# Kernel optimization log

Measured on AMD Instinct MI355X. Metric: run time of the kernel, lower is better.

Reference implementation:

```python
import jax, jax.numpy as jnp
import numpy as np

N = 50000      # nodes
E = 800000     # edges (avg degree 16)
D_IN = 128     # node_feature_dim
H = 256        # hidden_dim
EPS = 1e-5     # BatchNorm eps


def setup_inputs() -> dict:
    key = jax.random.key(0)
    ks = jax.random.split(key, 32)
    inp = {
        "x": jax.random.normal(ks[0], (N, D_IN), jnp.float32),
        "edge_index": jax.random.randint(ks[1], (2, E), 0, N, jnp.int32),
    }
    dims = [(D_IN, H), (H, H), (H, H)]
    k = 2
    for i, (din, dout) in enumerate(dims):
        s = 1.0 / np.sqrt(din)
        inp[f"Wl{i}"] = jax.random.uniform(ks[k], (din, dout), jnp.float32, -s, s); k += 1
        inp[f"bl{i}"] = jax.random.uniform(ks[k], (dout,), jnp.float32, -s, s); k += 1
        inp[f"Wr{i}"] = jax.random.uniform(ks[k], (din, dout), jnp.float32, -s, s); k += 1
        inp[f"g{i}"] = jnp.ones((dout,), jnp.float32)
        inp[f"b{i}"] = jnp.zeros((dout,), jnp.float32)
        inp[f"rm{i}"] = jax.random.normal(ks[k], (dout,), jnp.float32) * 0.1; k += 1
        inp[f"rv{i}"] = jax.random.uniform(ks[k], (dout,), jnp.float32, 0.5, 1.5); k += 1
    return inp


def _sage(x, src, dst, Wl, bl, Wr):
    # PyG SAGEConv (aggr='mean'): out = lin_l(mean_{j in N(i)} x_j) + lin_r(x_i)
    deg = jax.ops.segment_sum(jnp.ones((src.shape[0],), x.dtype), dst, num_segments=N)
    agg = jax.ops.segment_sum(x[src], dst, num_segments=N)  # [N, d_in]
    mean = agg / jnp.maximum(deg, 1.0)[:, None]
    return mean @ Wl + bl + x @ Wr


def _bn(x, g, b, rm, rv):
    # eval-mode BatchNorm1d with running stats
    return (x - rm) * (g * jax.lax.rsqrt(rv + EPS)) + b


def reference(x, edge_index,
              Wl0, bl0, Wr0, g0, b0, rm0, rv0,
              Wl1, bl1, Wr1, g1, b1, rm1, rv1,
              Wl2, bl2, Wr2, g2, b2, rm2, rv2):
    src, dst = edge_index[0], edge_index[1]
    h = jax.nn.relu(_bn(_sage(x, src, dst, Wl0, bl0, Wr0), g0, b0, rm0, rv0))
    h = jax.nn.relu(_bn(_sage(h, src, dst, Wl1, bl1, Wr1), g1, b1, rm1, rv1))
    h = _bn(_sage(h, src, dst, Wl2, bl2, Wr2), g2, b2, rm2, rv2)
    return h  # [N, H] node embeddings (dropout is identity in eval mode)
```

## Files before the change

kernel.cpp:

```cpp
#include <hip/hip_runtime.h>
#include <hip/hip_bf16.h>

#define NNODES 50000
#define NEDGES 800000
#define HID 256
#define BN_EPS 1e-5f
#define SCAN_B ((NNODES + 255) / 256)

typedef __attribute__((ext_vector_type(8))) short short8v;
typedef __attribute__((ext_vector_type(4))) float f32x4;
typedef __attribute__((ext_vector_type(2))) float f32x2;

__device__ inline void load_lds16(const void* g, void* l) {
    __builtin_amdgcn_global_load_lds(
        (const __attribute__((address_space(1))) unsigned int*)g,
        (__attribute__((address_space(3))) unsigned int*)l, 16, 0, 0);
}

__global__ void k_countrank(const int* __restrict__ ei, int* __restrict__ cnt,
                            int* __restrict__ rank, int nE) {
    int e = blockIdx.x * blockDim.x + threadIdx.x;
    if (e < nE) rank[e] = atomicAdd(&cnt[ei[nE + e]], 1);
}

__global__ void k_bsum(const int* __restrict__ cnt, int* __restrict__ loc,
                       int* __restrict__ bsum, int n) {
    __shared__ int sh[256];
    int tid = threadIdx.x;
    int i = blockIdx.x * 256 + tid;
    int v = (i < n) ? cnt[i] : 0;
    sh[tid] = v;
    __syncthreads();
    for (int off = 1; off < 256; off <<= 1) {
        int t = (tid >= off) ? sh[tid - off] : 0;
        __syncthreads();
        sh[tid] += t;
        __syncthreads();
    }
    if (i < n) loc[i] = sh[tid] - v;
    if (tid == 255) bsum[blockIdx.x] = sh[255];
}

__global__ void k_bscan(int* __restrict__ bsum, int nb) {
    __shared__ int sh[256];
    int tid = threadIdx.x;
    int v = (tid < nb) ? bsum[tid] : 0;
    sh[tid] = v;
    __syncthreads();
    for (int off = 1; off < 256; off <<= 1) {
        int t = (tid >= off) ? sh[tid - off] : 0;
        __syncthreads();
        sh[tid] += t;
        __syncthreads();
    }
    if (tid < nb) bsum[tid] = sh[tid] - v;
}

__global__ void k_addoff(const int* __restrict__ loc, const int* __restrict__ bsum,
                         int* __restrict__ rowptr, int n, int nE) {
    int i = blockIdx.x * 256 + threadIdx.x;
    if (i < n) rowptr[i] = loc[i] + bsum[blockIdx.x];
    if (i == 0) rowptr[n] = nE;
}

__global__ void k_fill2(const int* __restrict__ ei, const int* __restrict__ rowptr,
                        const int* __restrict__ rank, int* __restrict__ col, int nE) {
    int e = blockIdx.x * blockDim.x + threadIdx.x;
    if (e < nE) col[rowptr[ei[nE + e]] + rank[e]] = ei[e];
}

#define PREP_CAST 1600000
#define PREP_TR   327680
__global__ void k_prep(const float* __restrict__ x,
                       __hip_bfloat16* __restrict__ xb, unsigned char* __restrict__ x8,
                       const float* __restrict__ s0, const float* __restrict__ s1,
                       const float* __restrict__ s2, const float* __restrict__ s3,
                       const float* __restrict__ s4, const float* __restrict__ s5,
                       __hip_bfloat16* __restrict__ d0, __hip_bfloat16* __restrict__ d1,
                       __hip_bfloat16* __restrict__ d2, __hip_bfloat16* __restrict__ d3,
                       __hip_bfloat16* __restrict__ d4, __hip_bfloat16* __restrict__ d5,
                       int* __restrict__ cnt) {
    int f = blockIdx.x * blockDim.x + threadIdx.x;
    if (f < PREP_CAST) {
        float4 v = *(const float4*)(x + f * 4);
        union { uint2 u; unsigned short s[4]; } ob;
        ob.s[0] = __bfloat16_as_ushort(__float2bfloat16(v.x));
        ob.s[1] = __bfloat16_as_ushort(__float2bfloat16(v.y));
        ob.s[2] = __bfloat16_as_ushort(__float2bfloat16(v.z));
        ob.s[3] = __bfloat16_as_ushort(__float2bfloat16(v.w));
        *(uint2*)(xb + f * 4) = ob.u;
        int p = __builtin_amdgcn_cvt_pk_fp8_f32(v.x, v.y, 0, false);
        p = __builtin_amdgcn_cvt_pk_fp8_f32(v.z, v.w, p, true);
        *(int*)(x8 + f * 4) = p;
    } else if (f < PREP_CAST + PREP_TR) {
        int r = f - PREP_CAST;
        const float* src; __hip_bfloat16* dst; int K; int i;
        if (r < 65536) {
            K = 128;
            if (r < 32768) { src = s0; dst = d0; i = r; }
            else           { src = s1; dst = d1; i = r - 32768; }
        } else {
            K = 256;
            int q = r - 65536;
            int wsel = q >> 16;
            i = q & 65535;
            src = (wsel == 0) ? s2 : (wsel == 1) ? s3 : (wsel == 2) ? s4 : s5;
            dst = (wsel == 0) ? d2 : (wsel == 1) ? d3 : (wsel == 2) ? d4 : d5;
        }
        int k = i >> 8;
        int nn = i & 255;
        dst[nn * K + k] = __float2bfloat16(src[i]);
    } else {
        int i = f - PREP_CAST - PREP_TR;
        if (i < NNODES) cnt[i] = 0;
    }
}

template <int D, int U>
__global__ void k_meanf8(const unsigned char* __restrict__ x8,
                         const int* __restrict__ rowptr, const int* __restrict__ col,
                         __hip_bfloat16* __restrict__ mean, int n) {
    constexpr int CPL = D / 16;
    constexpr int R = 64 / CPL;
    int gw = (blockIdx.x * blockDim.x + threadIdx.x) >> 6;
    int lane = threadIdx.x & 63;
    if (gw >= n) return;
    int beg = rowptr[gw], end = rowptr[gw + 1];
    int sub = lane / CPL;
    int fpos = lane % CPL;
    const uint4* base = (const uint4*)x8;

    float acc[16];
#pragma unroll
    for (int j = 0; j < 16; j++) acc[j] = 0.f;

    for (int p0 = beg; p0 < end; p0 += U * R) {
        int idx[U]; bool ok[U];
#pragma unroll
        for (int u = 0; u < U; u++) {
            int p = p0 + u * R + sub;
            ok[u] = (p < end);
            idx[u] = ok[u] ? col[p] : 0;
        }
        uint4 v[U];
#pragma unroll
        for (int u = 0; u < U; u++) {
            uint4 t = {0u, 0u, 0u, 0u};
            if (ok[u]) t = base[(size_t)idx[u] * CPL + fpos];
            v[u] = t;
        }
#pragma unroll
        for (int u = 0; u < U; u++) {
            const unsigned int uu[4] = {v[u].x, v[u].y, v[u].z, v[u].w};
#pragma unroll
            for (int q = 0; q < 4; q++) {
                f32x2 lo = __builtin_amdgcn_cvt_pk_f32_fp8(uu[q], false);
                f32x2 hi = __builtin_amdgcn_cvt_pk_f32_fp8(uu[q], true);
                acc[4 * q + 0] += lo.x;
                acc[4 * q + 1] += lo.y;
                acc[4 * q + 2] += hi.x;
                acc[4 * q + 3] += hi.y;
            }
        }
    }

    if constexpr (R >= 8) {
#pragma unroll
        for (int j = 0; j < 16; j++) acc[j] += __shfl_xor(acc[j], 8, 64);
    }
#pragma unroll
    for (int j = 0; j < 16; j++) acc[j] += __shfl_xor(acc[j], 16, 64);
#pragma unroll
    for (int j = 0; j < 16; j++) acc[j] += __shfl_xor(acc[j], 32, 64);

    if (sub == 0) {
        float inv = (end > beg) ? 1.f / (float)(end - beg) : 0.f;
        union { uint4 v[2]; unsigned short s[16]; } o;
#pragma unroll
        for (int j = 0; j < 16; j++)
            o.s[j] = __bfloat16_as_ushort(__float2bfloat16(acc[j] * inv));
        uint4* dst = (uint4*)(mean + (size_t)gw * D + fpos * 16);
        dst[0] = o.v[0];
        dst[1] = o.v[1];
    }
}

template <int K, typename OutT, int RELU, int W8>
__launch_bounds__(256, 2)
__global__ void k_gemm2(const __hip_bfloat16* __restrict__ A1,
                        const __hip_bfloat16* __restrict__ A2,
                        const __hip_bfloat16* __restrict__ W1t,
                        const __hip_bfloat16* __restrict__ W2t,
                        const float* __restrict__ bl,
                        const float* __restrict__ g,
                        const float* __restrict__ bb,
                        const float* __restrict__ rm,
                        const float* __restrict__ rv,
                        OutT* __restrict__ out, unsigned char* __restrict__ out8,
                        int n) {
    __shared__ __hip_bfloat16 As1[128 * 32];
    __shared__ __hip_bfloat16 As2[128 * 32];
    __shared__ __hip_bfloat16 Bs1[256 * 32];
    __shared__ __hip_bfloat16 Bs2[256 * 32];
    int tid = threadIdx.x;
    int lane = tid & 63;
    int w = tid >> 6;
    int quad = lane >> 4;
    int ml = lane & 15;
    int rowBase = blockIdx.x * 128;
    int wr = w >> 1, wc = w & 1;

    f32x4 acc[4][8];
#pragma unroll
    for (int i = 0; i < 4; i++)
#pragma unroll
        for (int t = 0; t < 8; t++) acc[i][t] = {0.f, 0.f, 0.f, 0.f};

    int srow = tid >> 2;
    int sbyte = (tid & 3) * 16;

    for (int k0 = 0; k0 < K; k0 += 32) {
        __syncthreads();
#pragma unroll
        for (int h = 0; h < 2; h++) {
            int r = srow + h * 64;
            int grow = rowBase + r; if (grow >= n) grow = n - 1;
            load_lds16((const char*)(A1 + (size_t)grow * K + k0) + sbyte,
                       (char*)As1 + r * 64 + sbyte);
            load_lds16((const char*)(A2 + (size_t)grow * K + k0) + sbyte,
                       (char*)As2 + r * 64 + sbyte);
        }
#pragma unroll
        for (int h = 0; h < 4; h++) {
            int c = srow + h * 64;
            load_lds16((const char*)(W1t + (size_t)c * K + k0) + sbyte,
                       (char*)Bs1 + c * 64 + sbyte);
            load_lds16((const char*)(W2t + (size_t)c * K + k0) + sbyte,
                       (char*)Bs2 + c * 64 + sbyte);
        }
        __syncthreads();

        short8v af1[4], af2[4];
#pragma unroll
        for (int i = 0; i < 4; i++) {
            af1[i] = *(const short8v*)(As1 + (wr * 64 + i * 16 + ml) * 32 + quad * 8);
            af2[i] = *(const short8v*)(As2 + (wr * 64 + i * 16 + ml) * 32 + quad * 8);
        }
#pragma unroll
        for (int t = 0; t < 8; t++) {
            short8v bf1 = *(const short8v*)(Bs1 + (wc * 128 + t * 16 + ml) * 32 + quad * 8);
            short8v bf2 = *(const short8v*)(Bs2 + (wc * 128 + t * 16 + ml) * 32 + quad * 8);
#pragma unroll
            for (int i = 0; i < 4; i++) {
                acc[i][t] = __builtin_amdgcn_mfma_f32_16x16x32_bf16(af1[i], bf1, acc[i][t], 0, 0, 0);
                acc[i][t] = __builtin_amdgcn_mfma_f32_16x16x32_bf16(af2[i], bf2, acc[i][t], 0, 0, 0);
            }
        }
    }

#pragma unroll
    for (int t = 0; t < 8; t++) {
        int c = wc * 128 + t * 16 + ml;
        float sv = g[c] * rsqrtf(rv[c] + BN_EPS);
        float tv = (bl[c] - rm[c]) * sv + bb[c];
#pragma unroll
        for (int i = 0; i < 4; i++) {
            int row0 = rowBase + wr * 64 + i * 16 + quad * 4;
#pragma unroll
            for (int r = 0; r < 4; r++) {
                int row = row0 + r;
                if (row < n) {
                    float v = acc[i][t][r] * sv + tv;
                    if (RELU) v = fmaxf(v, 0.f);
                    if constexpr (sizeof(OutT) == 2)
                        out[(size_t)row * HID + c] = (OutT)__float2bfloat16(v);
                    else
                        out[(size_t)row * HID + c] = (OutT)v;
                    if constexpr (W8) {
                        int p = __builtin_amdgcn_cvt_pk_fp8_f32(v, v, 0, false);
                        out8[(size_t)row * HID + c] = (unsigned char)(p & 0xFF);
                    }
                }
            }
        }
    }
}

extern "C" void kernel_launch(void* const* d_in, const int* in_sizes, int n_in,
                              void* d_out, int out_size, void* d_ws, size_t ws_size,
                              hipStream_t stream) {
    const float* x = (const float*)d_in[0];
    const int* ei = (const int*)d_in[1];
    const float *Wl[3], *blv[3], *Wr[3], *g[3], *bb[3], *rm[3], *rv[3];
    for (int i = 0; i < 3; i++) {
        int b = 2 + i * 7;
        Wl[i]  = (const float*)d_in[b + 0];
        blv[i] = (const float*)d_in[b + 1];
        Wr[i]  = (const float*)d_in[b + 2];
        g[i]   = (const float*)d_in[b + 3];
        bb[i]  = (const float*)d_in[b + 4];
        rm[i]  = (const float*)d_in[b + 5];
        rv[i]  = (const float*)d_in[b + 6];
    }

    char* ob = (char*)d_out;
    __hip_bfloat16* xb = (__hip_bfloat16*)ob;
    __hip_bfloat16* h0 = (__hip_bfloat16*)(ob + (size_t)NNODES * 128 * 2);

    char* w = (char*)d_ws;
    size_t off = 0;
    auto alloc = [&](size_t bytes) {
        void* p = w + off;
        off += (bytes + 255) & ~(size_t)255;
        return p;
    };
    int* rowptr = (int*)alloc((NNODES + 1) * sizeof(int));
    int* cnt    = (int*)alloc(NNODES * sizeof(int));
    int* loc    = (int*)alloc(NNODES * sizeof(int));
    int* bsum   = (int*)alloc(SCAN_B * sizeof(int));
    int* rank   = (int*)alloc(NEDGES * sizeof(int));
    int* col    = (int*)alloc(NEDGES * sizeof(int));
    __hip_bfloat16* meanb = (__hip_bfloat16*)alloc((size_t)NNODES * HID * 2);
    __hip_bfloat16* h1    = (__hip_bfloat16*)alloc((size_t)NNODES * HID * 2);
    unsigned char* x8   = (unsigned char*)alloc((size_t)NNODES * 128);
    unsigned char* h0f8 = (unsigned char*)alloc((size_t)NNODES * HID);
    unsigned char* h1f8 = (unsigned char*)alloc((size_t)NNODES * HID);
    __hip_bfloat16* Wt[6];
    int Ks[6] = {128, 128, 256, 256, 256, 256};
    for (int i = 0; i < 6; i++) Wt[i] = (__hip_bfloat16*)alloc((size_t)Ks[i] * HID * 2);

    int prepTotal = PREP_CAST + PREP_TR + NNODES;
    k_prep<<<(prepTotal + 255) / 256, 256, 0, stream>>>(
        x, xb, x8, Wl[0], Wr[0], Wl[1], Wr[1], Wl[2], Wr[2],
        Wt[0], Wt[1], Wt[2], Wt[3], Wt[4], Wt[5], cnt);

    k_countrank<<<(NEDGES + 255) / 256, 256, 0, stream>>>(ei, cnt, rank, NEDGES);
    k_bsum<<<SCAN_B, 256, 0, stream>>>(cnt, loc, bsum, NNODES);
    k_bscan<<<1, 256, 0, stream>>>(bsum, SCAN_B);
    k_addoff<<<SCAN_B, 256, 0, stream>>>(loc, bsum, rowptr, NNODES, NEDGES);
    k_fill2<<<(NEDGES + 255) / 256, 256, 0, stream>>>(ei, rowptr, rank, col, NEDGES);

    int meanBlocks = (NNODES * 64 + 255) / 256;
    int gemmBlocks = (NNODES + 127) / 128;

    k_meanf8<128, 2><<<meanBlocks, 256, 0, stream>>>(x8, rowptr, col, meanb, NNODES);
    k_gemm2<128, __hip_bfloat16, 1, 1><<<gemmBlocks, 256, 0, stream>>>(meanb, xb, Wt[0], Wt[1],
        blv[0], g[0], bb[0], rm[0], rv[0], h0, h0f8, NNODES);

    k_meanf8<256, 4><<<meanBlocks, 256, 0, stream>>>(h0f8, rowptr, col, meanb, NNODES);
    k_gemm2<256, __hip_bfloat16, 1, 1><<<gemmBlocks, 256, 0, stream>>>(meanb, h0, Wt[2], Wt[3],
        blv[1], g[1], bb[1], rm[1], rv[1], h1, h1f8, NNODES);

    k_meanf8<256, 4><<<meanBlocks, 256, 0, stream>>>(h1f8, rowptr, col, meanb, NNODES);
    k_gemm2<256, float, 0, 0><<<gemmBlocks, 256, 0, stream>>>(meanb, h1, Wt[4], Wt[5],
        blv[2], g[2], bb[2], rm[2], rv[2], (float*)d_out, (unsigned char*)nullptr, NNODES);
}
```

Measured before the change: 378.7 us.

## Restructure dual GEMM: resident weight slice in LDS, direct A register loads, staged epilogue

The dual GEMM now gives each block a 256-row by 64-column output tile. The block loads the whole K-by-64 slice of both weight matrices into LDS once, so the K loop no longer re-stages weights with barriers. Activation fragments come straight from global memory into registers through a three-deep software prefetch, with no per-K-step syncthreads. The epilogue writes BN/ReLU results to an LDS scratch buffer, then emits vectorized 16-byte bf16/fp32 and 8-byte fp8 row stores. The cost is reading each activation row from four column-tile blocks instead of one, and a 64KB LDS footprint that may limit occupancy.

Result: slower. 415.3 us (+9.7%).

```diff
diff --git a/kernel.cpp b/kernel.cpp
--- a/kernel.cpp
+++ b/kernel.cpp
@@ -185,9 +185,9 @@
     }
 }
 
-template <int K, typename OutT, int RELU, int W8>
+template <int KH, typename OutT, int RELU, int W8>
 __launch_bounds__(256, 2)
-__global__ void k_gemm2(const __hip_bfloat16* __restrict__ A1,
+__global__ void k_gemm3(const __hip_bfloat16* __restrict__ A1,
                         const __hip_bfloat16* __restrict__ A2,
                         const __hip_bfloat16* __restrict__ W1t,
                         const __hip_bfloat16* __restrict__ W2t,
@@ -198,89 +198,122 @@
                         const float* __restrict__ rv,
                         OutT* __restrict__ out, unsigned char* __restrict__ out8,
                         int n) {
-    __shared__ __hip_bfloat16 As1[128 * 32];
-    __shared__ __hip_bfloat16 As2[128 * 32];
-    __shared__ __hip_bfloat16 Bs1[256 * 32];
-    __shared__ __hip_bfloat16 Bs2[256 * 32];
+    constexpr int NSTEP = KH / 16;
+    constexpr int K8TOT = KH / 4;
+    __shared__ uint4 ldsv[4096];
+    char* lds = (char*)ldsv;
     int tid = threadIdx.x;
-    int lane = tid & 63;
-    int w = tid >> 6;
-    int quad = lane >> 4;
-    int ml = lane & 15;
-    int rowBase = blockIdx.x * 128;
-    int wr = w >> 1, wc = w & 1;
-
-    f32x4 acc[4][8];
+    int rb = blockIdx.x >> 2, ct = blockIdx.x & 3;
+    int colbase = ct * 64;
+
+#pragma unroll
+    for (int it = 0; it < K8TOT / 4; it++) {
+        int j = tid + it * 256;
+        int k8 = j >> 6, c = j & 63;
+        const __hip_bfloat16* src =
+            (k8 < KH / 8) ? (W1t + (size_t)(colbase + c) * KH + k8 * 8)
+                          : (W2t + (size_t)(colbase + c) * KH + (k8 - KH / 8) * 8);
+        *(uint4*)(lds + (size_t)j * 16) = *(const uint4*)src;
+    }
+
+    int lane = tid & 63, wv = tid >> 6;
+    int quad = lane >> 4, ml = lane & 15;
+    int row0 = rb * 256 + wv * 64;
+
+    const short8v* p1[4];
+    const short8v* p2[4];
+#pragma unroll
+    for (int i = 0; i < 4; i++) {
+        int r = row0 + i * 16 + ml;
+        if (r > n - 1) r = n - 1;
+        p1[i] = (const short8v*)(A1 + (size_t)r * KH) + quad;
+        p2[i] = (const short8v*)(A2 + (size_t)r * KH) + quad;
+    }
+
+    f32x4 acc[4][4];
 #pragma unroll
     for (int i = 0; i < 4; i++)
 #pragma unroll
-        for (int t = 0; t < 8; t++) acc[i][t] = {0.f, 0.f, 0.f, 0.f};
-
-    int srow = tid >> 2;
-    int sbyte = (tid & 3) * 16;
-
-    for (int k0 = 0; k0 < K; k0 += 32) {
-        __syncthreads();
-#pragma unroll
-        for (int h = 0; h < 2; h++) {
-            int r = srow + h * 64;
-            int grow = rowBase + r; if (grow >= n) grow = n - 1;
-            load_lds16((const char*)(A1 + (size_t)grow * K + k0) + sbyte,
-                       (char*)As1 + r * 64 + sbyte);
-            load_lds16((const char*)(A2 + (size_t)grow * K + k0) + sbyte,
-                       (char*)As2 + r * 64 + sbyte);
-        }
-#pragma unroll
-        for (int h = 0; h < 4; h++) {
-            int c = srow + h * 64;
-            load_lds16((const char*)(W1t + (size_t)c * K + k0) + sbyte,
-                       (char*)Bs1 + c * 64 + sbyte);
-            load_lds16((const char*)(W2t + (size_t)c * K + k0) + sbyte,
-                       (char*)Bs2 + c * 64 + sbyte);
-        }
-        __syncthreads();
-
-        short8v af1[4], af2[4];
-#pragma unroll
-        for (int i = 0; i < 4; i++) {
-            af1[i] = *(const short8v*)(As1 + (wr * 64 + i * 16 + ml) * 32 + quad * 8);
-            af2[i] = *(const short8v*)(As2 + (wr * 64 + i * 16 + ml) * 32 + quad * 8);
-        }
-#pragma unroll
-        for (int t = 0; t < 8; t++) {
-            short8v bf1 = *(const short8v*)(Bs1 + (wc * 128 + t * 16 + ml) * 32 + quad * 8);
-            short8v bf2 = *(const short8v*)(Bs2 + (wc * 128 + t * 16 + ml) * 32 + quad * 8);
-#pragma unroll
-            for (int i = 0; i < 4; i++) {
-                acc[i][t] = __builtin_amdgcn_mfma_f32_16x16x32_bf16(af1[i], bf1, acc[i][t], 0, 0, 0);
-                acc[i][t] = __builtin_amdgcn_mfma_f32_16x16x32_bf16(af2[i], bf2, acc[i][t], 0, 0, 0);
-            }
-        }
-    }
-
-#pragma unroll
-    for (int t = 0; t < 8; t++) {
-        int c = wc * 128 + t * 16 + ml;
+        for (int t = 0; t < 4; t++) acc[i][t] = {0.f, 0.f, 0.f, 0.f};
+
+    short8v ab[3][4];
+#pragma unroll
+    for (int s = 0; s < 2; s++) {
+        const short8v* const* pp = (s < NSTEP / 2) ? p1 : p2;
+        int sh = (s < NSTEP / 2) ? s : s - NSTEP / 2;
+#pragma unroll
+        for (int i = 0; i < 4; i++) ab[s][i] = pp[i][sh * 4];
+    }
+    __syncthreads();
+
+#pragma unroll
+    for (int s = 0; s < NSTEP; s++) {
+        int sn = s + 2;
+        if (sn < NSTEP) {
+            const short8v* const* pp = (sn < NSTEP / 2) ? p1 : p2;
+            int sh = (sn < NSTEP / 2) ? sn : sn - NSTEP / 2;
+#pragma unroll
+            for (int i = 0; i < 4; i++) ab[sn % 3][i] = pp[i][sh * 4];
+        }
+        short8v bfr[4];
+#pragma unroll
+        for (int t = 0; t < 4; t++)
+            bfr[t] = *(const short8v*)(lds + ((size_t)((s * 4 + quad) * 64 + t * 16 + ml)) * 16);
+#pragma unroll
+        for (int t = 0; t < 4; t++)
+#pragma unroll
+            for (int i = 0; i < 4; i++)
+                acc[i][t] = __builtin_amdgcn_mfma_f32_16x16x32_bf16(
+                    ab[s % 3][i], bfr[t], acc[i][t], 0, 0, 0);
+    }
+
+    __syncthreads();
+    float* scr = (float*)(lds + wv * 16384);
+#pragma unroll
+    for (int t = 0; t < 4; t++) {
+        int c = colbase + t * 16 + ml;
         float sv = g[c] * rsqrtf(rv[c] + BN_EPS);
         float tv = (bl[c] - rm[c]) * sv + bb[c];
 #pragma unroll
-        for (int i = 0; i < 4; i++) {
-            int row0 = rowBase + wr * 64 + i * 16 + quad * 4;
+        for (int i = 0; i < 4; i++)
 #pragma unroll
             for (int r = 0; r < 4; r++) {
-                int row = row0 + r;
-                if (row < n) {
-                    float v = acc[i][t][r] * sv + tv;
-                    if (RELU) v = fmaxf(v, 0.f);
-                    if constexpr (sizeof(OutT) == 2)
-                        out[(size_t)row * HID + c] = (OutT)__float2bfloat16(v);
-                    else
-                        out[(size_t)row * HID + c] = (OutT)v;
-                    if constexpr (W8) {
-                        int p = __builtin_amdgcn_cvt_pk_fp8_f32(v, v, 0, false);
-                        out8[(size_t)row * HID + c] = (unsigned char)(p & 0xFF);
-                    }
-                }
+                float v = acc[i][t][r] * sv + tv;
+                if (RELU) v = fmaxf(v, 0.f);
+                scr[(i * 16 + quad * 4 + r) * 64 + t * 16 + ml] = v;
+            }
+    }
+    int rl8 = lane >> 3, c8 = (lane & 7) * 8;
+#pragma unroll
+    for (int p = 0; p < 8; p++) {
+        int rowl = p * 8 + rl8;
+        int row = row0 + rowl;
+        f32x4 v0 = *(const f32x4*)(scr + rowl * 64 + c8);
+        f32x4 v1 = *(const f32x4*)(scr + rowl * 64 + c8 + 4);
+        if (row < n) {
+            if constexpr (sizeof(OutT) == 2) {
+                union { uint4 u; unsigned short s[8]; } o;
+                o.s[0] = __bfloat16_as_ushort(__float2bfloat16(v0.x));
+                o.s[1] = __bfloat16_as_ushort(__float2bfloat16(v0.y));
+                o.s[2] = __bfloat16_as_ushort(__float2bfloat16(v0.z));
+                o.s[3] = __bfloat16_as_ushort(__float2bfloat16(v0.w));
+                o.s[4] = __bfloat16_as_ushort(__float2bfloat16(v1.x));
+                o.s[5] = __bfloat16_as_ushort(__float2bfloat16(v1.y));
+                o.s[6] = __bfloat16_as_ushort(__float2bfloat16(v1.z));
+                o.s[7] = __bfloat16_as_ushort(__float2bfloat16(v1.w));
+                *(uint4*)(out + (size_t)row * HID + colbase + c8) = o.u;
+            } else {
+                float* dst = (float*)out + (size_t)row * HID + colbase + c8;
+                *(f32x4*)dst = v0;
+                *(f32x4*)(dst + 4) = v1;
+            }
+            if constexpr (W8) {
+                int lo = __builtin_amdgcn_cvt_pk_fp8_f32(v0.x, v0.y, 0, false);
+                lo = __builtin_amdgcn_cvt_pk_fp8_f32(v0.z, v0.w, lo, true);
+                int hi = __builtin_amdgcn_cvt_pk_fp8_f32(v1.x, v1.y, 0, false);
+                hi = __builtin_amdgcn_cvt_pk_fp8_f32(v1.z, v1.w, hi, true);
+                uint2 u2 = {(unsigned)lo, (unsigned)hi};
+                *(uint2*)(out8 + (size_t)row * HID + colbase + c8) = u2;
             }
         }
     }
@@ -341,17 +374,17 @@
     k_fill2<<<(NEDGES + 255) / 256, 256, 0, stream>>>(ei, rowptr, rank, col, NEDGES);
 
     int meanBlocks = (NNODES * 64 + 255) / 256;
-    int gemmBlocks = (NNODES + 127) / 128;
+    int gemmBlocks = ((NNODES + 255) / 256) * 4;
 
     k_meanf8<128, 2><<<meanBlocks, 256, 0, stream>>>(x8, rowptr, col, meanb, NNODES);
-    k_gemm2<128, __hip_bfloat16, 1, 1><<<gemmBlocks, 256, 0, stream>>>(meanb, xb, Wt[0], Wt[1],
+    k_gemm3<128, __hip_bfloat16, 1, 1><<<gemmBlocks, 256, 0, stream>>>(meanb, xb, Wt[0], Wt[1],
         blv[0], g[0], bb[0], rm[0], rv[0], h0, h0f8, NNODES);
 
     k_meanf8<256, 4><<<meanBlocks, 256, 0, stream>>>(h0f8, rowptr, col, meanb, NNODES);
-    k_gemm2<256, __hip_bfloat16, 1, 1><<<gemmBlocks, 256, 0, stream>>>(meanb, h0, Wt[2], Wt[3],
+    k_gemm3<256, __hip_bfloat16, 1, 1><<<gemmBlocks, 256, 0, stream>>>(meanb, h0, Wt[2], Wt[3],
         blv[1], g[1], bb[1], rm[1], rv[1], h1, h1f8, NNODES);
 
     k_meanf8<256, 4><<<meanBlocks, 256, 0, stream>>>(h1f8, rowptr, col, meanb, NNODES);
-    k_gemm2<256, float, 0, 0><<<gemmBlocks, 256, 0, stream>>>(meanb, h1, Wt[4], Wt[5],
+    k_gemm3<256, float, 0, 0><<<gemmBlocks, 256, 0, stream>>>(meanb, h1, Wt[4], Wt[5],
         blv[2], g[2], bb[2], rm[2], rv[2], (float*)d_out, (unsigned char*)nullptr, NNODES);
 }
```
